# Optimization experiments

Hardware: AMD Instinct MI355X
Metric: run time of the kernel (lower is better)

Reference implementation:

```python
import jax, jax.numpy as jnp
import numpy as np

B, S, E, H, NQ, FF = 4, 1024, 256, 32, 8, 1024
DK = E // H  # 8, equals n_wires of the quantum attention layer
EPS = 1e-5


def layernorm(x, g, b):
    mu = jnp.mean(x, axis=-1, keepdims=True)
    var = jnp.mean(jnp.square(x - mu), axis=-1, keepdims=True)
    return (x - mu) * jax.lax.rsqrt(var + EPS) * g + b


def setup_inputs() -> dict:
    key = jax.random.key(0)
    ks = jax.random.split(key, 20)
    s = lambda n: 1.0 / np.sqrt(n)
    return {
        "x": jax.random.normal(ks[0], (B, S, E), dtype=jnp.float32),
        # quantum attention trainable RX angles (one per wire)
        "theta_attn": jax.random.uniform(ks[1], (DK,), minval=-np.pi, maxval=np.pi),
        # nn.MultiheadAttention packed in-proj and out-proj
        "w_in": jax.random.normal(ks[2], (3 * E, E)) * s(E),
        "b_in": jnp.zeros((3 * E,), jnp.float32),
        "w_out": jax.random.normal(ks[3], (E, E)) * s(E),
        "b_out": jnp.zeros((E,), jnp.float32),
        # combine linear
        "w_comb": jax.random.normal(ks[4], (E, E)) * s(E),
        "b_comb": jnp.zeros((E,), jnp.float32),
        # layernorms
        "g1": jnp.ones((E,), jnp.float32), "be1": jnp.zeros((E,), jnp.float32),
        "g2": jnp.ones((E,), jnp.float32), "be2": jnp.zeros((E,), jnp.float32),
        # FFN: input_proj, quantum RY angles, linear1, linear2
        "w_ip": jax.random.normal(ks[5], (NQ, E)) * s(E),
        "b_ip": jnp.zeros((NQ,), jnp.float32),
        "theta_ffn": jax.random.uniform(ks[6], (NQ,), minval=-np.pi, maxval=np.pi),
        "w1": jax.random.normal(ks[7], (FF, NQ)) * s(NQ),
        "b1": jnp.zeros((FF,), jnp.float32),
        "w2": jax.random.normal(ks[8], (E, FF)) * s(FF),
        "b2": jnp.zeros((E,), jnp.float32),
    }


def reference(x, theta_attn, w_in, b_in, w_out, b_out, w_comb, b_comb,
              g1, be1, g2, be2, w_ip, b_ip, theta_ffn, w1, b1, w2, b2):
    batch, seq, embed = x.shape
    # ---- QuantumAttention ----
    # per-head RX(x_i) encoding followed by trainable RX(theta_i): <Z_i> = cos(x_i + theta_i)
    xh = x.reshape(batch, seq, H, DK)            # [B,S,H,dk]
    q_out = jnp.cos(xh + theta_attn).reshape(batch, seq, embed)
    # standard multi-head self-attention on q_out (q=k=v)
    qkv = q_out @ w_in.T + b_in                  # [B,S,3E]
    q, k, v = jnp.split(qkv, 3, axis=-1)
    def heads(t):
        return t.reshape(batch, seq, H, DK).transpose(0, 2, 1, 3)  # [B,H,S,dk]
    q, k, v = heads(q), heads(k), heads(v)
    scores = jnp.einsum('bhqd,bhkd->bhqk', q, k) / np.sqrt(DK)
    attn = jax.nn.softmax(scores, axis=-1)
    ctx = jnp.einsum('bhqk,bhkd->bhqd', attn, v)
    ctx = ctx.transpose(0, 2, 1, 3).reshape(batch, seq, embed)
    attn_out = (ctx @ w_out.T + b_out) @ w_comb.T + b_comb
    # ---- residual + norm1 ----
    h = layernorm(x + attn_out, g1, be1)
    # ---- QuantumFeedForward ----
    proj = h @ w_ip.T + b_ip                     # [B,S,NQ]
    # RX(x) encoding then trainable RY(phi): <Z> = cos(phi) * cos(x)
    qf = jnp.cos(theta_ffn) * jnp.cos(proj)
    ffn_out = jax.nn.relu(qf @ w1.T + b1) @ w2.T + b2
    # ---- residual + norm2 ----
    return layernorm(h + ffn_out, g2, be2)
```

## Files before the change

### kernel.cpp

```cpp
#include <hip/hip_runtime.h>
#include <hip/hip_bf16.h>

#define B_  4
#define S_  1024
#define E_  256
#define H_  32
#define NQ_ 8
#define FF_ 1024
#define M_  (B_*S_)
#define QS  0.5100880289202462f
#define VSTRIDE 1036

typedef __attribute__((ext_vector_type(8))) short bf16x8;
typedef __attribute__((ext_vector_type(4))) short short4v;
typedef __attribute__((ext_vector_type(4))) float f32x4;

#if __has_builtin(__builtin_amdgcn_exp2f)
#define EXP2 __builtin_amdgcn_exp2f
#else
#define EXP2 exp2f
#endif

__device__ inline short f2bf(float f) {
    union { float f; unsigned u; } v; v.f = f;
    unsigned r = (v.u + 0x7fff + ((v.u >> 16) & 1)) >> 16;
    return (short)r;
}

__device__ inline float bf2f(ushort u_) {
    union { unsigned u; float f; } c; c.u = ((unsigned)u_) << 16; return c.f;
}

__device__ inline unsigned pk2(float a, float b) {
    __hip_bfloat162 h = __float22bfloat162_rn(make_float2(a, b));
    union { __hip_bfloat162 h; unsigned u; } c; c.h = h;
    return c.u;
}

__global__ __launch_bounds__(256) void d1_kernel(
        const float* __restrict__ x, const float* __restrict__ theta_attn,
        const float* __restrict__ w_in, const float* __restrict__ b_in,
        const float* __restrict__ w_out, const float* __restrict__ w_comb,
        const float* __restrict__ b_out, const float* __restrict__ b_comb,
        const float* __restrict__ w2,
        ushort* __restrict__ qkv_bf, ushort* __restrict__ weff_bf,
        float* __restrict__ beff, ushort* __restrict__ w2_bf) {
    __shared__ ushort As[128 * 64];
    __shared__ ushort Bs[64 * 64];
    __shared__ float red[4];
    int bid = blockIdx.x, tid = threadIdx.x;

    if (bid >= 392) {
        if (bid < 648) {
            int i = bid - 392;
            float p = w_comb[(size_t)i * 256 + tid] * b_out[tid];
#pragma unroll
            for (int o = 32; o > 0; o >>= 1) p += __shfl_xor(p, o);
            if ((tid & 63) == 0) red[tid >> 6] = p;
            __syncthreads();
            if (tid == 0) beff[i] = red[0] + red[1] + red[2] + red[3] + b_comb[i];
        } else {
            int i = (bid - 648) * 256 + tid;
            float4 v = ((const float4*)w2)[i];
            short4v o = {f2bf(v.x), f2bf(v.y), f2bf(v.z), f2bf(v.w)};
            ((short4v*)w2_bf)[i] = o;
        }
        return;
    }

    bool isW = bid >= 384;
    int bm, bn;
    if (!isW) { bm = (bid / 12) * 128; bn = (bid % 12) * 64; }
    else      { int t = bid - 384; bm = (t >> 2) * 128; bn = (t & 3) * 64; }

    int w = tid >> 6, l = tid & 63, lq = l & 15, hi = l >> 4;
    int wm = w & 1, wn = w >> 1;
    f32x4 acc[4][2] = {};
    int srow = tid >> 3;
    int sk = (tid & 7) * 8;
    float wscale = isW ? 1.f : ((bn < 256) ? QS : 1.f);
    float th[8];
    if (!isW) {
#pragma unroll
        for (int j = 0; j < 8; ++j) th[j] = theta_attn[j];
    }

    for (int k0 = 0; k0 < 256; k0 += 64) {
        __syncthreads();
        if (!isW) {
#pragma unroll
            for (int it = 0; it < 4; ++it) {
                int row = it * 32 + srow;
                const float* xp = x + (size_t)(bm + row) * 256 + k0 + sk;
                float4 a = *(const float4*)xp;
                float4 b = *(const float4*)(xp + 4);
                bf16x8 o;
                o[0] = f2bf(__cosf(a.x + th[0]));
                o[1] = f2bf(__cosf(a.y + th[1]));
                o[2] = f2bf(__cosf(a.z + th[2]));
                o[3] = f2bf(__cosf(a.w + th[3]));
                o[4] = f2bf(__cosf(b.x + th[4]));
                o[5] = f2bf(__cosf(b.y + th[5]));
                o[6] = f2bf(__cosf(b.z + th[6]));
                o[7] = f2bf(__cosf(b.w + th[7]));
                *(bf16x8*)((char*)As + row * 128 + ((sk * 2) ^ ((row & 7) << 4))) = o;
            }
#pragma unroll
            for (int it = 0; it < 2; ++it) {
                int row = it * 32 + srow;
                const float* wp = w_in + (size_t)(bn + row) * 256 + k0 + sk;
                float4 a = *(const float4*)wp;
                float4 b = *(const float4*)(wp + 4);
                bf16x8 o;
                o[0] = f2bf(a.x * wscale); o[1] = f2bf(a.y * wscale);
                o[2] = f2bf(a.z * wscale); o[3] = f2bf(a.w * wscale);
                o[4] = f2bf(b.x * wscale); o[5] = f2bf(b.y * wscale);
                o[6] = f2bf(b.z * wscale); o[7] = f2bf(b.w * wscale);
                *(bf16x8*)((char*)Bs + row * 128 + ((sk * 2) ^ ((row & 7) << 4))) = o;
            }
        } else {
#pragma unroll
            for (int it = 0; it < 4; ++it) {
                int row = it * 32 + srow;
                const float* wp = w_comb + (size_t)(bm + row) * 256 + k0 + sk;
                float4 a = *(const float4*)wp;
                float4 b = *(const float4*)(wp + 4);
                bf16x8 o;
                o[0] = f2bf(a.x); o[1] = f2bf(a.y); o[2] = f2bf(a.z); o[3] = f2bf(a.w);
                o[4] = f2bf(b.x); o[5] = f2bf(b.y); o[6] = f2bf(b.z); o[7] = f2bf(b.w);
                *(bf16x8*)((char*)As + row * 128 + ((sk * 2) ^ ((row & 7) << 4))) = o;
            }
            int nl = tid & 63, kg = tid >> 6;
#pragma unroll
            for (int kk = 0; kk < 16; ++kk) {
                int kb = (kg * 16 + kk) * 2;
                float v = w_out[(size_t)(k0 + kg * 16 + kk) * 256 + bn + nl];
                *(ushort*)((char*)Bs + nl * 128 + (kb ^ ((nl & 7) << 4))) = (ushort)f2bf(v);
            }
        }
        __syncthreads();
#pragma unroll
        for (int kk = 0; kk < 2; ++kk) {
            bf16x8 af[4], bfr[2];
#pragma unroll
            for (int mf = 0; mf < 4; ++mf) {
                int row = wm * 64 + mf * 16 + lq;
                af[mf] = *(const bf16x8*)((const char*)As + row * 128 +
                                          ((kk * 64 + hi * 16) ^ ((row & 7) << 4)));
            }
#pragma unroll
            for (int nf = 0; nf < 2; ++nf) {
                int row = wn * 32 + nf * 16 + lq;
                bfr[nf] = *(const bf16x8*)((const char*)Bs + row * 128 +
                                           ((kk * 64 + hi * 16) ^ ((row & 7) << 4)));
            }
#pragma unroll
            for (int mf = 0; mf < 4; ++mf)
#pragma unroll
                for (int nf = 0; nf < 2; ++nf)
                    acc[mf][nf] = __builtin_amdgcn_mfma_f32_16x16x32_bf16(af[mf], bfr[nf], acc[mf][nf], 0, 0, 0);
        }
    }
    ushort* Cp = isW ? weff_bf : qkv_bf;
    int Nd = isW ? 256 : 768;
#pragma unroll
    for (int mf = 0; mf < 4; ++mf)
#pragma unroll
        for (int nf = 0; nf < 2; ++nf) {
            int n = bn + wn * 32 + nf * 16 + lq;
            float bv = isW ? 0.f : b_in[n] * wscale;
#pragma unroll
            for (int r = 0; r < 4; ++r) {
                int m = bm + wm * 64 + mf * 16 + hi * 4 + r;
                Cp[(size_t)m * Nd + n] = (ushort)f2bf(acc[mf][nf][r] + bv);
            }
        }
}

__global__ __launch_bounds__(256, 4) void attn_mfma_kernel(const ushort* __restrict__ qkv,
                                                           ushort* __restrict__ ctx) {
    __shared__ ushort ks[S_ * 8];
    __shared__ ushort vt[9 * VSTRIDE + 4];
    int qt = blockIdx.x, h = blockIdx.y, b = blockIdx.z;
    int tid = threadIdx.x;
    const ushort* base = qkv + (size_t)b * S_ * (3 * E_) + h * 8;

    for (int i = tid; i < S_; i += 256) {
        const ushort* rp = base + (size_t)i * (3 * E_);
        bf16x8 kv = *(const bf16x8*)(rp + E_);
        bf16x8 vv = *(const bf16x8*)(rp + 2 * E_);
        *(bf16x8*)&ks[i * 8] = kv;
        int kf = (i >> 4) & 3, hh = (i >> 2) & 3, s = i & 3;
        int pv = (i & ~63) + ((kf >> 1) << 5) + (hh << 3) + ((kf & 1) << 2) + s;
#pragma unroll
        for (int d = 0; d < 8; ++d) vt[d * VSTRIDE + pv] = vv[d];
        vt[8 * VSTRIDE + pv] = 0x3F80;
    }
    __syncthreads();

    int w = tid >> 6, l = tid & 63, lq = l & 15, g = l >> 4;

    bf16x8 qfrag[2];
#pragma unroll
    for (int qf = 0; qf < 2; ++qf) {
        bf16x8 qv = {};
        if (g == 0)
            qv = *(const bf16x8*)(base + (size_t)(qt * 128 + w * 32 + qf * 16 + lq) * (3 * E_));
        qfrag[qf] = qv;
    }

    f32x4 ctxa[2] = {{0.f,0.f,0.f,0.f},{0.f,0.f,0.f,0.f}};
    const f32x4 zf = {0.f, 0.f, 0.f, 0.f};

#pragma unroll 2
    for (int kt = 0; kt < 16; ++kt) {
        bf16x8 kfrag[4];
#pragma unroll
        for (int kf = 0; kf < 4; ++kf) {
            bf16x8 kv = {};
            if (g == 0) kv = *(bf16x8*)&ks[(kt * 64 + kf * 16 + lq) * 8];
            kfrag[kf] = kv;
        }
        bf16x8 vf0 = *(bf16x8*)&vt[lq * VSTRIDE + kt * 64 + g * 8];
        bf16x8 vf1 = *(bf16x8*)&vt[lq * VSTRIDE + kt * 64 + 32 + g * 8];
        __builtin_amdgcn_s_setprio(1);
#pragma unroll
        for (int qf = 0; qf < 2; ++qf) {
            f32x4 st[4];
#pragma unroll
            for (int kf = 0; kf < 4; ++kf)
                st[kf] = __builtin_amdgcn_mfma_f32_16x16x32_bf16(kfrag[kf], qfrag[qf], zf, 0, 0, 0);
            union { unsigned u[4]; bf16x8 v; } p0, p1;
            p0.u[0] = pk2(EXP2(st[0][0]), EXP2(st[0][1]));
            p0.u[1] = pk2(EXP2(st[0][2]), EXP2(st[0][3]));
            p0.u[2] = pk2(EXP2(st[1][0]), EXP2(st[1][1]));
            p0.u[3] = pk2(EXP2(st[1][2]), EXP2(st[1][3]));
            p1.u[0] = pk2(EXP2(st[2][0]), EXP2(st[2][1]));
            p1.u[1] = pk2(EXP2(st[2][2]), EXP2(st[2][3]));
            p1.u[2] = pk2(EXP2(st[3][0]), EXP2(st[3][1]));
            p1.u[3] = pk2(EXP2(st[3][2]), EXP2(st[3][3]));
            ctxa[qf] = __builtin_amdgcn_mfma_f32_16x16x32_bf16(p0.v, vf0, ctxa[qf], 0, 0, 0);
            ctxa[qf] = __builtin_amdgcn_mfma_f32_16x16x32_bf16(p1.v, vf1, ctxa[qf], 0, 0, 0);
        }
        __builtin_amdgcn_s_setprio(0);
    }

#pragma unroll
    for (int qf = 0; qf < 2; ++qf) {
        int src = (l & 48) + 8;
        float s0 = __shfl(ctxa[qf][0], src);
        float s1 = __shfl(ctxa[qf][1], src);
        float s2 = __shfl(ctxa[qf][2], src);
        float s3 = __shfl(ctxa[qf][3], src);
        if (lq < 8) {
            float i0 = __builtin_amdgcn_rcpf(s0);
            float i1 = __builtin_amdgcn_rcpf(s1);
            float i2 = __builtin_amdgcn_rcpf(s2);
            float i3 = __builtin_amdgcn_rcpf(s3);
            int tok = b * S_ + qt * 128 + w * 32 + qf * 16 + g * 4;
            ushort* cp = ctx + (size_t)tok * E_ + h * 8 + lq;
            cp[0]      = (ushort)f2bf(ctxa[qf][0] * i0);
            cp[E_]     = (ushort)f2bf(ctxa[qf][1] * i1);
            cp[2 * E_] = (ushort)f2bf(ctxa[qf][2] * i2);
            cp[3 * E_] = (ushort)f2bf(ctxa[qf][3] * i3);
        }
    }
}

__global__ __launch_bounds__(256) void d34_kernel(
        const ushort* __restrict__ ctx, const ushort* __restrict__ weff,
        const float* __restrict__ beff, const float* __restrict__ x,
        const float* __restrict__ g1, const float* __restrict__ be1,
        const float* __restrict__ w_ip, const float* __restrict__ b_ip,
        const float* __restrict__ theta_ffn,
        const float* __restrict__ w1, const float* __restrict__ b1,
        const ushort* __restrict__ w2b, const float* __restrict__ b2,
        const float* __restrict__ g2, const float* __restrict__ be2,
        float* __restrict__ out) {
    __shared__ float hs[16 * 260];
    __shared__ float qfl[16 * 8];
    __shared__ ushort ts[16 * 1024];
    __shared__ float red[2][16][4];
    int tid = threadIdx.x;
    int bm = blockIdx.x * 16;
    int wn = tid >> 6, l = tid & 63, lq = l & 15, hi = l >> 4;

    f32x4 acc[4] = {};
#pragma unroll
    for (int k0 = 0; k0 < 256; k0 += 64) {
#pragma unroll
        for (int kk = 0; kk < 2; ++kk) {
            bf16x8 af = *(const bf16x8*)(ctx + (size_t)(bm + lq) * 256 + k0 + kk * 32 + hi * 8);
#pragma unroll
            for (int nf = 0; nf < 4; ++nf) {
                int rb = wn * 64 + nf * 16 + lq;
                bf16x8 bf_ = *(const bf16x8*)(weff + (size_t)rb * 256 + k0 + kk * 32 + hi * 8);
                acc[nf] = __builtin_amdgcn_mfma_f32_16x16x32_bf16(af, bf_, acc[nf], 0, 0, 0);
            }
        }
    }

    float vv[4][4];
    float rs[4] = {}, rq[4] = {};
#pragma unroll
    for (int nf = 0; nf < 4; ++nf) {
        int n = wn * 64 + nf * 16 + lq;
        float bv = beff[n];
#pragma unroll
        for (int r = 0; r < 4; ++r) {
            int m = bm + hi * 4 + r;
            float val = acc[nf][r] + bv + x[(size_t)m * 256 + n];
            vv[nf][r] = val;
            rs[r] += val;
            rq[r] += val * val;
        }
    }
#pragma unroll
    for (int o = 1; o < 16; o <<= 1)
#pragma unroll
        for (int r = 0; r < 4; ++r) {
            rs[r] += __shfl_xor(rs[r], o);
            rq[r] += __shfl_xor(rq[r], o);
        }
    if (lq == 0) {
#pragma unroll
        for (int r = 0; r < 4; ++r) {
            red[0][hi * 4 + r][wn] = rs[r];
            red[1][hi * 4 + r][wn] = rq[r];
        }
    }
    __syncthreads();
#pragma unroll
    for (int r = 0; r < 4; ++r) {
        int row = hi * 4 + r;
        float st_ = red[0][row][0] + red[0][row][1] + red[0][row][2] + red[0][row][3];
        float sq_ = red[1][row][0] + red[1][row][1] + red[1][row][2] + red[1][row][3];
        float mu = st_ * (1.f / 256.f);
        float var = sq_ * (1.f / 256.f) - mu * mu;
        rs[r] = mu;
        rq[r] = rsqrtf(var + 1e-5f);
    }
#pragma unroll
    for (int nf = 0; nf < 4; ++nf) {
        int n = wn * 64 + nf * 16 + lq;
        float gn = g1[n], bn_ = be1[n];
#pragma unroll
        for (int r = 0; r < 4; ++r) {
            int row = hi * 4 + r;
            hs[row * 260 + n] = (vv[nf][r] - rs[r]) * rq[r] * gn + bn_;
        }
    }
    __syncthreads();

    if (tid < 128) {
        int tok = tid >> 3, wq = tid & 7;
        const float* wip = w_ip + wq * 256;
        float pr = 0.f;
#pragma unroll
        for (int c = 0; c < 64; ++c) {
            float4 hv = *(const float4*)&hs[tok * 260 + c * 4];
            float4 wv = *(const float4*)(wip + c * 4);
            pr += hv.x * wv.x + hv.y * wv.y + hv.z * wv.z + hv.w * wv.w;
        }
        qfl[tok * 8 + wq] = __cosf(theta_ffn[wq]) * __cosf(pr + b_ip[wq]);
    }
    __syncthreads();

    {
        int row = tid & 15, fb = tid >> 4;
        float q[8];
#pragma unroll
        for (int k = 0; k < 8; ++k) q[k] = qfl[row * 8 + k];
#pragma unroll
        for (int j8 = 0; j8 < 8; ++j8) {
            int f0 = fb * 64 + j8 * 8;
            bf16x8 o;
#pragma unroll
            for (int j = 0; j < 8; ++j) {
                const float* wp = w1 + (size_t)(f0 + j) * 8;
                float4 wa = *(const float4*)wp;
                float4 wb = *(const float4*)(wp + 4);
                float s = b1[f0 + j]
                        + q[0] * wa.x + q[1] * wa.y + q[2] * wa.z + q[3] * wa.w
                        + q[4] * wb.x + q[5] * wb.y + q[6] * wb.z + q[7] * wb.w;
                o[j] = f2bf(fmaxf(s, 0.f));
            }
            *(bf16x8*)((char*)ts + row * 2048 + ((f0 * 2) ^ ((row & 7) << 4))) = o;
        }
    }
    __syncthreads();

    f32x4 acc2[4] = {};
#pragma unroll 4
    for (int k0 = 0; k0 < 1024; k0 += 64) {
#pragma unroll
        for (int kk = 0; kk < 2; ++kk) {
            bf16x8 af = *(const bf16x8*)((const char*)ts + lq * 2048 +
                                         ((k0 * 2 + kk * 64 + hi * 16) ^ ((lq & 7) << 4)));
#pragma unroll
            for (int nf = 0; nf < 4; ++nf) {
                int rb = wn * 64 + nf * 16 + lq;
                bf16x8 bf_ = *(const bf16x8*)(w2b + (size_t)rb * 1024 + k0 + kk * 32 + hi * 8);
                acc2[nf] = __builtin_amdgcn_mfma_f32_16x16x32_bf16(af, bf_, acc2[nf], 0, 0, 0);
            }
        }
    }

    float rs2[4] = {}, rq2[4] = {};
#pragma unroll
    for (int nf = 0; nf < 4; ++nf) {
        int n = wn * 64 + nf * 16 + lq;
        float bv = b2[n];
#pragma unroll
        for (int r = 0; r < 4; ++r) {
            int row = hi * 4 + r;
            float val = acc2[nf][r] + bv + hs[row * 260 + n];
            vv[nf][r] = val;
            rs2[r] += val;
            rq2[r] += val * val;
        }
    }
#pragma unroll
    for (int o = 1; o < 16; o <<= 1)
#pragma unroll
        for (int r = 0; r < 4; ++r) {
            rs2[r] += __shfl_xor(rs2[r], o);
            rq2[r] += __shfl_xor(rq2[r], o);
        }
    __syncthreads();
    if (lq == 0) {
#pragma unroll
        for (int r = 0; r < 4; ++r) {
            red[0][hi * 4 + r][wn] = rs2[r];
            red[1][hi * 4 + r][wn] = rq2[r];
        }
    }
    __syncthreads();
#pragma unroll
    for (int r = 0; r < 4; ++r) {
        int row = hi * 4 + r;
        float st_ = red[0][row][0] + red[0][row][1] + red[0][row][2] + red[0][row][3];
        float sq_ = red[1][row][0] + red[1][row][1] + red[1][row][2] + red[1][row][3];
        float mu = st_ * (1.f / 256.f);
        float var = sq_ * (1.f / 256.f) - mu * mu;
        rs2[r] = mu;
        rq2[r] = rsqrtf(var + 1e-5f);
    }
#pragma unroll
    for (int nf = 0; nf < 4; ++nf) {
        int n = wn * 64 + nf * 16 + lq;
        float gn = g2[n], bn_ = be2[n];
#pragma unroll
        for (int r = 0; r < 4; ++r) {
            int row = hi * 4 + r;
            out[(size_t)(bm + row) * 256 + n] =
                (vv[nf][r] - rs2[r]) * rq2[r] * gn + bn_;
        }
    }
}

extern "C" void kernel_launch(void* const* d_in, const int* in_sizes, int n_in,
                              void* d_out, int out_size, void* d_ws, size_t ws_size,
                              hipStream_t stream) {
    const float* x          = (const float*)d_in[0];
    const float* theta_attn = (const float*)d_in[1];
    const float* w_in       = (const float*)d_in[2];
    const float* b_in       = (const float*)d_in[3];
    const float* w_out      = (const float*)d_in[4];
    const float* b_out      = (const float*)d_in[5];
    const float* w_comb     = (const float*)d_in[6];
    const float* b_comb     = (const float*)d_in[7];
    const float* g1         = (const float*)d_in[8];
    const float* be1        = (const float*)d_in[9];
    const float* g2         = (const float*)d_in[10];
    const float* be2        = (const float*)d_in[11];
    const float* w_ip       = (const float*)d_in[12];
    const float* b_ip       = (const float*)d_in[13];
    const float* theta_ffn  = (const float*)d_in[14];
    const float* w1         = (const float*)d_in[15];
    const float* b1         = (const float*)d_in[16];
    const float* w2         = (const float*)d_in[17];
    const float* b2         = (const float*)d_in[18];
    float* out = (float*)d_out;

    char* wsb = (char*)d_ws;
    ushort* qkv_bf  = (ushort*)(wsb);
    ushort* ctx_bf  = (ushort*)(wsb + (6u << 20));
    ushort* weff_bf = (ushort*)(wsb + (8u << 20));
    ushort* w2_bf   = (ushort*)(wsb + (8u << 20) + 131072);
    float*  beff    = (float*)(wsb + (9u << 20));

    d1_kernel<<<904, 256, 0, stream>>>(x, theta_attn, w_in, b_in, w_out, w_comb,
                                       b_out, b_comb, w2, qkv_bf, weff_bf, beff, w2_bf);
    attn_mfma_kernel<<<dim3(S_ / 128, H_, B_), 256, 0, stream>>>(qkv_bf, ctx_bf);
    d34_kernel<<<M_ / 16, 256, 0, stream>>>(ctx_bf, weff_bf, beff, x, g1, be1,
                                            w_ip, b_ip, theta_ffn, w1, b1,
                                            w2_bf, b2, g2, be2, out);
}
```

Measured before the change: 181.2 us.

## Precompute cos-encoded q_out in separate kernel and pre-convert w1 to bf16

Moves the cos(x+theta) encoding out of the QKV GEMM tile loader into a standalone kernel that writes a bf16 q_out buffer. Previously each output-column block recomputed the cosines for its A tile, 12 times per row. The d1 kernel now loads bf16 directly, and w1 is converted to bf16 alongside w2 so the FFN first layer reads half the bytes. This costs an extra kernel launch plus a 2 MB intermediate write and read, and w1 loses precision by being rounded to bf16.

```diff
diff --git a/kernel.cpp b/kernel.cpp
--- a/kernel.cpp
+++ b/kernel.cpp
@@ -37,14 +37,33 @@
     return c.u;
 }
 
+__global__ __launch_bounds__(256) void qout_kernel(const float* __restrict__ x,
+                                                   const float* __restrict__ theta,
+                                                   ushort* __restrict__ qout) {
+    int i = blockIdx.x * 256 + threadIdx.x;
+    float4 a = ((const float4*)x)[i * 2];
+    float4 b = ((const float4*)x)[i * 2 + 1];
+    bf16x8 o;
+    o[0] = f2bf(__cosf(a.x + theta[0]));
+    o[1] = f2bf(__cosf(a.y + theta[1]));
+    o[2] = f2bf(__cosf(a.z + theta[2]));
+    o[3] = f2bf(__cosf(a.w + theta[3]));
+    o[4] = f2bf(__cosf(b.x + theta[4]));
+    o[5] = f2bf(__cosf(b.y + theta[5]));
+    o[6] = f2bf(__cosf(b.z + theta[6]));
+    o[7] = f2bf(__cosf(b.w + theta[7]));
+    *(bf16x8*)(qout + (size_t)i * 8) = o;
+}
+
 __global__ __launch_bounds__(256) void d1_kernel(
-        const float* __restrict__ x, const float* __restrict__ theta_attn,
-        const float* __restrict__ w_in, const float* __restrict__ b_in,
+        const ushort* __restrict__ qout, const float* __restrict__ w_in,
+        const float* __restrict__ b_in,
         const float* __restrict__ w_out, const float* __restrict__ w_comb,
         const float* __restrict__ b_out, const float* __restrict__ b_comb,
-        const float* __restrict__ w2,
+        const float* __restrict__ w2, const float* __restrict__ w1,
         ushort* __restrict__ qkv_bf, ushort* __restrict__ weff_bf,
-        float* __restrict__ beff, ushort* __restrict__ w2_bf) {
+        float* __restrict__ beff, ushort* __restrict__ w2_bf,
+        ushort* __restrict__ w1_bf) {
     __shared__ ushort As[128 * 64];
     __shared__ ushort Bs[64 * 64];
     __shared__ float red[4];
@@ -59,11 +78,16 @@
             if ((tid & 63) == 0) red[tid >> 6] = p;
             __syncthreads();
             if (tid == 0) beff[i] = red[0] + red[1] + red[2] + red[3] + b_comb[i];
-        } else {
+        } else if (bid < 904) {
             int i = (bid - 648) * 256 + tid;
             float4 v = ((const float4*)w2)[i];
             short4v o = {f2bf(v.x), f2bf(v.y), f2bf(v.z), f2bf(v.w)};
             ((short4v*)w2_bf)[i] = o;
+        } else {
+            int i = (bid - 904) * 256 + tid;
+            float4 v = ((const float4*)w1)[i];
+            short4v o = {f2bf(v.x), f2bf(v.y), f2bf(v.z), f2bf(v.w)};
+            ((short4v*)w1_bf)[i] = o;
         }
         return;
     }
@@ -79,11 +103,6 @@
     int srow = tid >> 3;
     int sk = (tid & 7) * 8;
     float wscale = isW ? 1.f : ((bn < 256) ? QS : 1.f);
-    float th[8];
-    if (!isW) {
-#pragma unroll
-        for (int j = 0; j < 8; ++j) th[j] = theta_attn[j];
-    }
 
     for (int k0 = 0; k0 < 256; k0 += 64) {
         __syncthreads();
@@ -91,19 +110,8 @@
 #pragma unroll
             for (int it = 0; it < 4; ++it) {
                 int row = it * 32 + srow;
-                const float* xp = x + (size_t)(bm + row) * 256 + k0 + sk;
-                float4 a = *(const float4*)xp;
-                float4 b = *(const float4*)(xp + 4);
-                bf16x8 o;
-                o[0] = f2bf(__cosf(a.x + th[0]));
-                o[1] = f2bf(__cosf(a.y + th[1]));
-                o[2] = f2bf(__cosf(a.z + th[2]));
-                o[3] = f2bf(__cosf(a.w + th[3]));
-                o[4] = f2bf(__cosf(b.x + th[4]));
-                o[5] = f2bf(__cosf(b.y + th[5]));
-                o[6] = f2bf(__cosf(b.z + th[6]));
-                o[7] = f2bf(__cosf(b.w + th[7]));
-                *(bf16x8*)((char*)As + row * 128 + ((sk * 2) ^ ((row & 7) << 4))) = o;
+                bf16x8 v = *(const bf16x8*)(qout + (size_t)(bm + row) * 256 + k0 + sk);
+                *(bf16x8*)((char*)As + row * 128 + ((sk * 2) ^ ((row & 7) << 4))) = v;
             }
 #pragma unroll
             for (int it = 0; it < 2; ++it) {
@@ -273,7 +281,7 @@
         const float* __restrict__ g1, const float* __restrict__ be1,
         const float* __restrict__ w_ip, const float* __restrict__ b_ip,
         const float* __restrict__ theta_ffn,
-        const float* __restrict__ w1, const float* __restrict__ b1,
+        const ushort* __restrict__ w1b, const float* __restrict__ b1,
         const ushort* __restrict__ w2b, const float* __restrict__ b2,
         const float* __restrict__ g2, const float* __restrict__ be2,
         float* __restrict__ out) {
@@ -377,12 +385,10 @@
             bf16x8 o;
 #pragma unroll
             for (int j = 0; j < 8; ++j) {
-                const float* wp = w1 + (size_t)(f0 + j) * 8;
-                float4 wa = *(const float4*)wp;
-                float4 wb = *(const float4*)(wp + 4);
-                float s = b1[f0 + j]
-                        + q[0] * wa.x + q[1] * wa.y + q[2] * wa.z + q[3] * wa.w
-                        + q[4] * wb.x + q[5] * wb.y + q[6] * wb.z + q[7] * wb.w;
+                bf16x8 wv = *(const bf16x8*)(w1b + (size_t)(f0 + j) * 8);
+                float s = b1[f0 + j];
+#pragma unroll
+                for (int k = 0; k < 8; ++k) s += q[k] * bf2f((ushort)wv[k]);
                 o[j] = f2bf(fmaxf(s, 0.f));
             }
             *(bf16x8*)((char*)ts + row * 2048 + ((f0 * 2) ^ ((row & 7) << 4))) = o;
@@ -489,11 +495,15 @@
     ushort* weff_bf = (ushort*)(wsb + (8u << 20));
     ushort* w2_bf   = (ushort*)(wsb + (8u << 20) + 131072);
     float*  beff    = (float*)(wsb + (9u << 20));
-
-    d1_kernel<<<904, 256, 0, stream>>>(x, theta_attn, w_in, b_in, w_out, w_comb,
-                                       b_out, b_comb, w2, qkv_bf, weff_bf, beff, w2_bf);
+    ushort* w1_bf   = (ushort*)(wsb + (9u << 20) + 4096);
+    ushort* qout_bf = (ushort*)(wsb + (10u << 20));
+
+    qout_kernel<<<512, 256, 0, stream>>>(x, theta_attn, qout_bf);
+    d1_kernel<<<912, 256, 0, stream>>>(qout_bf, w_in, b_in, w_out, w_comb,
+                                       b_out, b_comb, w2, w1,
+                                       qkv_bf, weff_bf, beff, w2_bf, w1_bf);
     attn_mfma_kernel<<<dim3(S_ / 128, H_, B_), 256, 0, stream>>>(qkv_bf, ctx_bf);
     d34_kernel<<<M_ / 16, 256, 0, stream>>>(ctx_bf, weff_bf, beff, x, g1, be1,
-                                            w_ip, b_ip, theta_ffn, w1, b1,
+                                            w_ip, b_ip, theta_ffn, w1_bf, b1,
                                             w2_bf, b2, g2, be2, out);
 }
```

New measurement: 185.1 us. 2.2% more time.
